# Kernel tuning notes

Measured on AMD Instinct MI355X. Metric: run time of the kernel, lower is better.

The kernel has to match this reference:

```python
import math
import jax, jax.numpy as jnp
import numpy as np

EMBED_DIM = 512
NUM_HEADS = 8
PROJ_DIM = EMBED_DIM // NUM_HEADS
ATTN_WINDOW = 5
HALF_WINDOW = (ATTN_WINDOW - 1) // 2  # 2
ATTN_PARAM = 1.0
ATTN_DISPLACEMENT = 1
# per-head positions: ['center','left','right','center'] repeated to 8 heads (synst repeats short lists)
HEAD_SHIFTS = np.array([0, -ATTN_DISPLACEMENT, ATTN_DISPLACEMENT, 0] * 2, dtype=np.int32)


def _xavier(key, shape):
    fan_in, fan_out = shape[1], shape[0]
    bound = math.sqrt(6.0 / (fan_in + fan_out))
    return jax.random.uniform(key, shape, jnp.float32, -bound, bound)


def setup_inputs() -> dict:
    key = jax.random.key(0)
    k1, k2, k3, k4, k5 = jax.random.split(key, 5)
    B, S, E = 8, 4096, EMBED_DIM
    return {
        "values": jax.random.normal(k1, (B, S, E), jnp.float32),
        "keys": jax.random.normal(k2, (B, S, E), jnp.float32),
        "queries": jax.random.normal(k3, (B, S, E), jnp.float32),
        "input_weights": _xavier(k4, (E, E)),        # value projection (attn_weights=1, non-learned type)
        "out_proj_w": _xavier(k5, (E, E)),           # output_projection.weight (bias=False)
    }


def reference(values, keys, queries, input_weights, out_proj_w):
    # keys/queries are unused by the hard-coded 'normal' attention path (no QK^T)
    B, S, E = values.shape
    H, Dh, hw, W = NUM_HEADS, PROJ_DIM, HALF_WINDOW, ATTN_WINDOW

    # value projection + head split: [B,S,E] -> [B,H,S,Dh]
    v = values @ input_weights.T
    v = v.reshape(B, S, H, Dh).transpose(0, 2, 1, 3)

    # fixed Gaussian filter over relative distances [-hw, hw] (unnormalized pdf, as in the source)
    dist = jnp.arange(-hw, hw + 1, dtype=jnp.float32)
    filt = (1.0 / (ATTN_PARAM * math.sqrt(2.0 * math.pi))) * jnp.exp(-0.5 * (dist / ATTN_PARAM) ** 2)  # [W]

    shifts = jnp.asarray(HEAD_SHIFTS)            # [H] per-head center displacement
    P = hw + int(np.max(np.abs(HEAD_SHIFTS)))    # pad so all gathers are in range
    vp = jnp.pad(v, ((0, 0), (0, 0), (P, P), (0, 0)))  # [B,H,S+2P,Dh]

    h_ar = jnp.arange(H)[:, None]                # [H,1]
    pos = jnp.arange(S)[None, :]                 # [1,S]
    out = jnp.zeros_like(v)
    for j in range(W):                           # tiny fixed window loop (W=5)
        idx = pos + P + shifts[:, None] + (j - hw)   # [H,S]
        out = out + filt[j] * vp[:, h_ar, idx, :]    # [B,H,S,Dh]

    out = out.transpose(0, 2, 1, 3).reshape(B, S, E)
    return out @ out_proj_w.T
```

## Files before the change

kernel.cpp:

```cpp
#include <hip/hip_runtime.h>
#include <hip/hip_bf16.h>
#include <stdint.h>

typedef __bf16 bf16;
typedef __bf16 bf16x8 __attribute__((ext_vector_type(8)));
typedef float  f32x4  __attribute__((ext_vector_type(4)));

#define BM 128
#define BN 128
#define BK 32
#define E  512
#define SB 4112
#define M1 (8 * SB)
#define M2 32768

__device__ __forceinline__ void gl_lds_16(const bf16* g, bf16* l) {
    __builtin_amdgcn_global_load_lds(
        (__attribute__((address_space(1))) void*)g,
        (__attribute__((address_space(3))) void*)l,
        16, 0, 0);
}

__global__ __launch_bounds__(256)
void gemm_bt_bf16(const bf16* __restrict__ A, const bf16* __restrict__ Bm,
                  bf16* __restrict__ C, int M, int N, int K)
{
    __shared__ bf16 As[BM * BK];
    __shared__ bf16 Bs[BN * BK];

    const int tid  = threadIdx.x;
    const int bm   = blockIdx.x;
    const int bn   = blockIdx.y;
    const int wave = tid >> 6;
    const int lane = tid & 63;
    const int wm   = wave >> 1;
    const int wn   = wave & 1;

    const int srow = tid >> 2;
    const int scol = (tid & 3) << 3;
    const size_t a_off = (size_t)(bm * BM + srow) * K + scol;
    const size_t b_off = (size_t)(bn * BN + srow) * K + scol;
    const int    l_off = srow * BK + scol;

    f32x4 acc[4][4] = {};
    const int fr = lane & 15;
    const int ks = (lane >> 4) << 3;

    for (int k0 = 0; k0 < K; k0 += BK) {
        gl_lds_16(A  + a_off + k0,                  As + l_off);
        gl_lds_16(A  + a_off + (size_t)64 * K + k0, As + l_off + 64 * BK);
        gl_lds_16(Bm + b_off + k0,                  Bs + l_off);
        gl_lds_16(Bm + b_off + (size_t)64 * K + k0, Bs + l_off + 64 * BK);
        __syncthreads();

        bf16x8 af[4], bfr[4];
#pragma unroll
        for (int i = 0; i < 4; ++i) {
            af[i]  = *(const bf16x8*)(As + (wm * 64 + i * 16 + fr) * BK + ks);
            bfr[i] = *(const bf16x8*)(Bs + (wn * 64 + i * 16 + fr) * BK + ks);
        }
#pragma unroll
        for (int i = 0; i < 4; ++i)
#pragma unroll
            for (int j = 0; j < 4; ++j)
                acc[i][j] = __builtin_amdgcn_mfma_f32_16x16x32_bf16(af[i], bfr[j], acc[i][j], 0, 0, 0);
        __syncthreads();
    }

    const int crow = (lane >> 4) << 2;
    const int ccol = lane & 15;
    const int row0 = bm * BM + wm * 64 + crow;
    const int col0 = bn * BN + wn * 64 + ccol;
#pragma unroll
    for (int i = 0; i < 4; ++i)
#pragma unroll
        for (int j = 0; j < 4; ++j)
#pragma unroll
            for (int r = 0; r < 4; ++r)
                C[(size_t)(row0 + i * 16 + r) * N + (col0 + j * 16)] = (bf16)acc[i][j][r];
}

__global__ __launch_bounds__(256)
void gemm2_gather(const bf16* __restrict__ P, const bf16* __restrict__ Bm,
                  float* __restrict__ C)
{
    __shared__ bf16 As[BM * BK];
    __shared__ bf16 Bs[BN * BK];

    const int tid  = threadIdx.x;
    const int bm   = blockIdx.x;
    const int bn   = blockIdx.y;
    const int wave = tid >> 6;
    const int lane = tid & 63;
    const int wm   = wave >> 1;
    const int wn   = wave & 1;

    const int srow = tid >> 2;
    const int scol = (tid & 3) << 3;

    const int m0 = bm * BM + srow;
    const int m1 = m0 + 64;
    const int prow0 = (m0 >> 12) * SB + (m0 & 4095) + 1;
    const int prow1 = (m1 >> 12) * SB + (m1 & 4095) + 1;

    const size_t b_off = (size_t)(bn * BN + srow) * E + scol;
    const int    l_off = srow * BK + scol;

    f32x4 acc[4][4] = {};
    const int fr = lane & 15;
    const int ks = (lane >> 4) << 3;

    for (int k0 = 0; k0 < E; k0 += BK) {
        const int h3 = (k0 >> 6) & 3;
        const int sh = (h3 == 1) ? -1 : (h3 == 2) ? 1 : 0;
        gl_lds_16(P + (size_t)(prow0 + sh) * E + scol + k0, As + l_off);
        gl_lds_16(P + (size_t)(prow1 + sh) * E + scol + k0, As + l_off + 64 * BK);
        gl_lds_16(Bm + b_off + k0,                          Bs + l_off);
        gl_lds_16(Bm + b_off + (size_t)64 * E + k0,         Bs + l_off + 64 * BK);
        __syncthreads();

        bf16x8 af[4], bfr[4];
#pragma unroll
        for (int i = 0; i < 4; ++i) {
            af[i]  = *(const bf16x8*)(As + (wm * 64 + i * 16 + fr) * BK + ks);
            bfr[i] = *(const bf16x8*)(Bs + (wn * 64 + i * 16 + fr) * BK + ks);
        }
#pragma unroll
        for (int i = 0; i < 4; ++i)
#pragma unroll
            for (int j = 0; j < 4; ++j)
                acc[i][j] = __builtin_amdgcn_mfma_f32_16x16x32_bf16(af[i], bfr[j], acc[i][j], 0, 0, 0);
        __syncthreads();
    }

    const int crow = (lane >> 4) << 2;
    const int ccol = lane & 15;
    const int row0 = bm * BM + wm * 64 + crow;
    const int col0 = bn * BN + wn * 64 + ccol;
#pragma unroll
    for (int i = 0; i < 4; ++i)
#pragma unroll
        for (int j = 0; j < 4; ++j)
#pragma unroll
            for (int r = 0; r < 4; ++r)
                C[(size_t)(row0 + i * 16 + r) * E + (col0 + j * 16)] = acc[i][j][r];
}

__global__ __launch_bounds__(256)
void prefilter(const float* __restrict__ vals, bf16* __restrict__ vg)
{
    const int idx = blockIdx.x * 256 + threadIdx.x;
    const int e8  = idx & 63;
    const int m   = idx >> 6;
    const int b   = m / SB;
    const int r   = m - b * SB;

    const float filt[5] = {0.05399096651318806f, 0.24197072451914337f,
                           0.3989422804014327f,
                           0.24197072451914337f, 0.05399096651318806f};
    float acc[8] = {0.f, 0.f, 0.f, 0.f, 0.f, 0.f, 0.f, 0.f};
    if (r < 4098) {
#pragma unroll
        for (int j = 0; j < 5; ++j) {
            const int sp = r - 3 + j;
            if (sp >= 0 && sp < 4096) {
                const f32x4* p = (const f32x4*)(vals + ((size_t)(b * 4096 + sp)) * E + e8 * 8);
                f32x4 x0 = p[0], x1 = p[1];
                const float w = filt[j];
                acc[0] += w * x0[0]; acc[1] += w * x0[1];
                acc[2] += w * x0[2]; acc[3] += w * x0[3];
                acc[4] += w * x1[0]; acc[5] += w * x1[1];
                acc[6] += w * x1[2]; acc[7] += w * x1[3];
            }
        }
    }
    bf16x8 o;
#pragma unroll
    for (int d = 0; d < 8; ++d) o[d] = (bf16)acc[d];
    *((bf16x8*)vg + idx) = o;
}

__global__ __launch_bounds__(256)
void cvt_weights(const float* __restrict__ w_in, const float* __restrict__ w_out,
                 bf16* __restrict__ win_b, bf16* __restrict__ wout_b)
{
    const int i = blockIdx.x * 256 + threadIdx.x;
    const int half = (E * E) / 8;
    const float* src = (i < half) ? w_in : w_out;
    bf16* dst        = (i < half) ? win_b : wout_b;
    const int k = (i < half) ? i : i - half;
    const f32x4* p = (const f32x4*)src + 2 * (size_t)k;
    f32x4 a = p[0], bq = p[1];
    bf16x8 o;
    o[0] = (bf16)a[0]; o[1] = (bf16)a[1]; o[2] = (bf16)a[2]; o[3] = (bf16)a[3];
    o[4] = (bf16)bq[0]; o[5] = (bf16)bq[1]; o[6] = (bf16)bq[2]; o[7] = (bf16)bq[3];
    *((bf16x8*)dst + k) = o;
}

extern "C" void kernel_launch(void* const* d_in, const int* in_sizes, int n_in,
                              void* d_out, int out_size, void* d_ws, size_t ws_size,
                              hipStream_t stream)
{
    const float* values = (const float*)d_in[0];
    const float* w_in   = (const float*)d_in[3];
    const float* w_out  = (const float*)d_in[4];
    float* out = (float*)d_out;

    bf16* win_b  = (bf16*)d_ws;
    bf16* wout_b = win_b + E * E;
    bf16* vg     = wout_b + E * E;
    bf16* Pbuf   = vg + (size_t)M1 * E;

    cvt_weights<<<(2 * E * E / 8) / 256, 256, 0, stream>>>(w_in, w_out, win_b, wout_b);
    prefilter<<<(size_t)M1 * 64 / 256, 256, 0, stream>>>(values, vg);

    dim3 g1(M1 / BM, E / BN);
    gemm_bt_bf16<<<g1, 256, 0, stream>>>(vg, win_b, Pbuf, M1, E, E);

    dim3 g2(M2 / BM, E / BN);
    gemm2_gather<<<g2, 256, 0, stream>>>(Pbuf, wout_b, out);
}
```

Measured before the change: 257.0 us.

## Widen GEMM K-tile with XOR-swizzled LDS, raster grid, and reuse rows in prefilter

Both GEMMs now use a K-tile of 64 with an XOR-swizzled shared-memory layout, which halves the number of barrier-synchronised loop iterations and is meant to avoid LDS bank conflicts on the fragment reads. The grid is flattened so that the four N-tiles of one M-block are launched next to each other, which should keep the A tile hot in L2. The prefilter kernel now has each thread produce 8 consecutive output rows from 12 input rows instead of reading 5 rows per output row, cutting redundant global loads. The trade-off is more registers per thread in the prefilter and larger LDS tiles in the GEMMs, which could lower occupancy.

Measured after the change: 242.4 us. 5.7% less time.

```diff
diff --git a/kernel.cpp b/kernel.cpp
--- a/kernel.cpp
+++ b/kernel.cpp
@@ -8,7 +8,7 @@
 
 #define BM 128
 #define BN 128
-#define BK 32
+#define BK 64
 #define E  512
 #define SB 4112
 #define M1 (8 * SB)
@@ -29,41 +29,49 @@
     __shared__ bf16 Bs[BN * BK];
 
     const int tid  = threadIdx.x;
-    const int bm   = blockIdx.x;
-    const int bn   = blockIdx.y;
+    const int id   = blockIdx.x;
+    const int bm   = id >> 2;
+    const int bn   = id & 3;
     const int wave = tid >> 6;
     const int lane = tid & 63;
     const int wm   = wave >> 1;
     const int wn   = wave & 1;
 
-    const int srow = tid >> 2;
-    const int scol = (tid & 3) << 3;
+    const int srow = tid >> 3;
+    const int scol = (((tid & 7) ^ (srow & 7)) << 3);
     const size_t a_off = (size_t)(bm * BM + srow) * K + scol;
     const size_t b_off = (size_t)(bn * BN + srow) * K + scol;
-    const int    l_off = srow * BK + scol;
+    const int    l_off = tid * 8;
 
     f32x4 acc[4][4] = {};
     const int fr = lane & 15;
-    const int ks = (lane >> 4) << 3;
+    const int q  = lane >> 4;
 
     for (int k0 = 0; k0 < K; k0 += BK) {
-        gl_lds_16(A  + a_off + k0,                  As + l_off);
-        gl_lds_16(A  + a_off + (size_t)64 * K + k0, As + l_off + 64 * BK);
-        gl_lds_16(Bm + b_off + k0,                  Bs + l_off);
-        gl_lds_16(Bm + b_off + (size_t)64 * K + k0, Bs + l_off + 64 * BK);
-        __syncthreads();
-
-        bf16x8 af[4], bfr[4];
-#pragma unroll
-        for (int i = 0; i < 4; ++i) {
-            af[i]  = *(const bf16x8*)(As + (wm * 64 + i * 16 + fr) * BK + ks);
-            bfr[i] = *(const bf16x8*)(Bs + (wn * 64 + i * 16 + fr) * BK + ks);
-        }
-#pragma unroll
-        for (int i = 0; i < 4; ++i)
-#pragma unroll
-            for (int j = 0; j < 4; ++j)
-                acc[i][j] = __builtin_amdgcn_mfma_f32_16x16x32_bf16(af[i], bfr[j], acc[i][j], 0, 0, 0);
+#pragma unroll
+        for (int c = 0; c < 4; ++c) {
+            gl_lds_16(A  + a_off + (size_t)(c * 32) * K + k0, As + c * 2048 + l_off);
+            gl_lds_16(Bm + b_off + (size_t)(c * 32) * K + k0, Bs + c * 2048 + l_off);
+        }
+        __syncthreads();
+
+#pragma unroll
+        for (int t = 0; t < 2; ++t) {
+            bf16x8 af[4], bfr[4];
+#pragma unroll
+            for (int i = 0; i < 4; ++i) {
+                const int Ra = wm * 64 + i * 16 + fr;
+                const int Rb = wn * 64 + i * 16 + fr;
+                const int c  = t * 4 + q;
+                af[i]  = *(const bf16x8*)(As + Ra * BK + ((c ^ (Ra & 7)) << 3));
+                bfr[i] = *(const bf16x8*)(Bs + Rb * BK + ((c ^ (Rb & 7)) << 3));
+            }
+#pragma unroll
+            for (int i = 0; i < 4; ++i)
+#pragma unroll
+                for (int j = 0; j < 4; ++j)
+                    acc[i][j] = __builtin_amdgcn_mfma_f32_16x16x32_bf16(af[i], bfr[j], acc[i][j], 0, 0, 0);
+        }
         __syncthreads();
     }
 
@@ -88,48 +96,52 @@
     __shared__ bf16 Bs[BN * BK];
 
     const int tid  = threadIdx.x;
-    const int bm   = blockIdx.x;
-    const int bn   = blockIdx.y;
+    const int id   = blockIdx.x;
+    const int bm   = id >> 2;
+    const int bn   = id & 3;
     const int wave = tid >> 6;
     const int lane = tid & 63;
     const int wm   = wave >> 1;
     const int wn   = wave & 1;
 
-    const int srow = tid >> 2;
-    const int scol = (tid & 3) << 3;
-
-    const int m0 = bm * BM + srow;
-    const int m1 = m0 + 64;
-    const int prow0 = (m0 >> 12) * SB + (m0 & 4095) + 1;
-    const int prow1 = (m1 >> 12) * SB + (m1 & 4095) + 1;
-
+    const int srow = tid >> 3;
+    const int scol = (((tid & 7) ^ (srow & 7)) << 3);
     const size_t b_off = (size_t)(bn * BN + srow) * E + scol;
-    const int    l_off = srow * BK + scol;
+    const int    l_off = tid * 8;
 
     f32x4 acc[4][4] = {};
     const int fr = lane & 15;
-    const int ks = (lane >> 4) << 3;
+    const int q  = lane >> 4;
 
     for (int k0 = 0; k0 < E; k0 += BK) {
         const int h3 = (k0 >> 6) & 3;
         const int sh = (h3 == 1) ? -1 : (h3 == 2) ? 1 : 0;
-        gl_lds_16(P + (size_t)(prow0 + sh) * E + scol + k0, As + l_off);
-        gl_lds_16(P + (size_t)(prow1 + sh) * E + scol + k0, As + l_off + 64 * BK);
-        gl_lds_16(Bm + b_off + k0,                          Bs + l_off);
-        gl_lds_16(Bm + b_off + (size_t)64 * E + k0,         Bs + l_off + 64 * BK);
-        __syncthreads();
-
-        bf16x8 af[4], bfr[4];
-#pragma unroll
-        for (int i = 0; i < 4; ++i) {
-            af[i]  = *(const bf16x8*)(As + (wm * 64 + i * 16 + fr) * BK + ks);
-            bfr[i] = *(const bf16x8*)(Bs + (wn * 64 + i * 16 + fr) * BK + ks);
-        }
-#pragma unroll
-        for (int i = 0; i < 4; ++i)
-#pragma unroll
-            for (int j = 0; j < 4; ++j)
-                acc[i][j] = __builtin_amdgcn_mfma_f32_16x16x32_bf16(af[i], bfr[j], acc[i][j], 0, 0, 0);
+#pragma unroll
+        for (int c = 0; c < 4; ++c) {
+            const int m = bm * BM + c * 32 + srow;
+            const int prow = (m >> 12) * SB + (m & 4095) + 1 + sh;
+            gl_lds_16(P  + (size_t)prow * E + k0 + scol,          As + c * 2048 + l_off);
+            gl_lds_16(Bm + b_off + (size_t)(c * 32) * E + k0,     Bs + c * 2048 + l_off);
+        }
+        __syncthreads();
+
+#pragma unroll
+        for (int t = 0; t < 2; ++t) {
+            bf16x8 af[4], bfr[4];
+#pragma unroll
+            for (int i = 0; i < 4; ++i) {
+                const int Ra = wm * 64 + i * 16 + fr;
+                const int Rb = wn * 64 + i * 16 + fr;
+                const int c  = t * 4 + q;
+                af[i]  = *(const bf16x8*)(As + Ra * BK + ((c ^ (Ra & 7)) << 3));
+                bfr[i] = *(const bf16x8*)(Bs + Rb * BK + ((c ^ (Rb & 7)) << 3));
+            }
+#pragma unroll
+            for (int i = 0; i < 4; ++i)
+#pragma unroll
+                for (int j = 0; j < 4; ++j)
+                    acc[i][j] = __builtin_amdgcn_mfma_f32_16x16x32_bf16(af[i], bfr[j], acc[i][j], 0, 0, 0);
+        }
         __syncthreads();
     }
 
@@ -149,35 +161,50 @@
 __global__ __launch_bounds__(256)
 void prefilter(const float* __restrict__ vals, bf16* __restrict__ vg)
 {
-    const int idx = blockIdx.x * 256 + threadIdx.x;
-    const int e8  = idx & 63;
-    const int m   = idx >> 6;
-    const int b   = m / SB;
-    const int r   = m - b * SB;
+    const int tid  = threadIdx.x;
+    const int e8   = tid & 63;
+    const int gidx = blockIdx.x * 4 + (tid >> 6);
+    const int m0   = gidx << 3;
+    const int b    = m0 / SB;
+    const int r0   = m0 - b * SB;
 
     const float filt[5] = {0.05399096651318806f, 0.24197072451914337f,
                            0.3989422804014327f,
                            0.24197072451914337f, 0.05399096651318806f};
-    float acc[8] = {0.f, 0.f, 0.f, 0.f, 0.f, 0.f, 0.f, 0.f};
-    if (r < 4098) {
-#pragma unroll
-        for (int j = 0; j < 5; ++j) {
-            const int sp = r - 3 + j;
-            if (sp >= 0 && sp < 4096) {
-                const f32x4* p = (const f32x4*)(vals + ((size_t)(b * 4096 + sp)) * E + e8 * 8);
-                f32x4 x0 = p[0], x1 = p[1];
-                const float w = filt[j];
-                acc[0] += w * x0[0]; acc[1] += w * x0[1];
-                acc[2] += w * x0[2]; acc[3] += w * x0[3];
-                acc[4] += w * x1[0]; acc[5] += w * x1[1];
-                acc[6] += w * x1[2]; acc[7] += w * x1[3];
+
+    float acc[8][8];
+#pragma unroll
+    for (int t = 0; t < 8; ++t)
+#pragma unroll
+        for (int d = 0; d < 8; ++d) acc[t][d] = 0.f;
+
+    const float* bbase = vals + (size_t)b * 4096 * E + e8 * 8;
+#pragma unroll
+    for (int u = 0; u < 12; ++u) {
+        const int sp = r0 - 3 + u;
+        if (sp >= 0 && sp < 4096) {
+            const f32x4* p = (const f32x4*)(bbase + (size_t)sp * E);
+            const f32x4 x0 = p[0], x1 = p[1];
+            const float x[8] = {x0[0], x0[1], x0[2], x0[3],
+                                x1[0], x1[1], x1[2], x1[3]};
+#pragma unroll
+            for (int t = 0; t < 8; ++t) {
+                const int j = u - t;
+                if (j >= 0 && j < 5) {
+                    const float w = filt[j];
+#pragma unroll
+                    for (int d = 0; d < 8; ++d) acc[t][d] += w * x[d];
+                }
             }
         }
     }
-    bf16x8 o;
-#pragma unroll
-    for (int d = 0; d < 8; ++d) o[d] = (bf16)acc[d];
-    *((bf16x8*)vg + idx) = o;
+#pragma unroll
+    for (int t = 0; t < 8; ++t) {
+        bf16x8 o;
+#pragma unroll
+        for (int d = 0; d < 8; ++d) o[d] = (bf16)acc[t][d];
+        *((bf16x8*)vg + (size_t)(m0 + t) * 64 + e8) = o;
+    }
 }
 
 __global__ __launch_bounds__(256)
@@ -212,11 +239,8 @@
     bf16* Pbuf   = vg + (size_t)M1 * E;
 
     cvt_weights<<<(2 * E * E / 8) / 256, 256, 0, stream>>>(w_in, w_out, win_b, wout_b);
-    prefilter<<<(size_t)M1 * 64 / 256, 256, 0, stream>>>(values, vg);
-
-    dim3 g1(M1 / BM, E / BN);
-    gemm_bt_bf16<<<g1, 256, 0, stream>>>(vg, win_b, Pbuf, M1, E, E);
-
-    dim3 g2(M2 / BM, E / BN);
-    gemm2_gather<<<g2, 256, 0, stream>>>(Pbuf, wout_b, out);
-}
+    prefilter<<<M1 / 8 / 4, 256, 0, stream>>>(values, vg);
+
+    gemm_bt_bf16<<<(M1 / BM) * 4, 256, 0, stream>>>(vg, win_b, Pbuf, M1, E, E);
+    gemm2_gather<<<(M2 / BM) * 4, 256, 0, stream>>>(Pbuf, wout_b, out);
+}
```
